# Kernel optimization log

Measured on AMD Instinct MI355X. Metric: run time of the kernel, lower is better.

## Reference

```python
import jax, jax.numpy as jnp
import numpy as np

N_HEAD = 16
N_KV_HEAD = 4
HEAD_DIM = 128
RMS_EPS = 1.1920928955078125e-07  # torch float32 eps used by F.rms_norm default


def apply_rotary_emb(x, cos, sin):
    # x: [B,T,H,D]; cos/sin: [1,T,1,D/2]
    d = x.shape[-1] // 2
    x1, x2 = x[..., :d], x[..., d:]
    return jnp.concatenate([x1 * cos + x2 * sin, -x1 * sin + x2 * cos], axis=-1)


def rms_norm(x):
    return x * jax.lax.rsqrt(jnp.mean(x * x, axis=-1, keepdims=True) + RMS_EPS)


def setup_inputs() -> dict:
    key = jax.random.key(0)
    ks = jax.random.split(key, 7)
    B, T, C = 2, 2048, 2048
    return {
        "x": jax.random.normal(ks[0], (B, T, C), jnp.float32),
        "cos": jax.random.normal(ks[1], (1, T, 1, HEAD_DIM // 2), jnp.float32),
        "sin": jax.random.normal(ks[2], (1, T, 1, HEAD_DIM // 2), jnp.float32),
        "wq": jax.random.normal(ks[3], (C, N_HEAD * HEAD_DIM), jnp.float32) * 0.02,
        "wk": jax.random.normal(ks[4], (C, N_KV_HEAD * HEAD_DIM), jnp.float32) * 0.02,
        "wv": jax.random.normal(ks[5], (C, N_KV_HEAD * HEAD_DIM), jnp.float32) * 0.02,
        "wo": jax.random.normal(ks[6], (C, C), jnp.float32) * 0.02,
        "window_size": 512,
    }


def reference(x, cos, sin, wq, wk, wv, wo, window_size):
    B, T, C = x.shape
    H, KV, D = N_HEAD, N_KV_HEAD, HEAD_DIM
    rep = H // KV
    q = (x @ wq).reshape(B, T, H, D)
    k = (x @ wk).reshape(B, T, KV, D)
    v = (x @ wv).reshape(B, T, KV, D)
    q = rms_norm(apply_rotary_emb(q, cos, sin))
    k = rms_norm(apply_rotary_emb(k, cos, sin))
    # GQA: group query heads by kv head instead of materializing expanded K/V
    qg = q.reshape(B, T, KV, rep, D)
    scale = 1.0 / np.sqrt(D)
    scores = jnp.einsum('btkrd,bskd->bkrts', qg, k) * scale  # [B,KV,rep,T,S]
    row = jnp.arange(T)[:, None]
    col = jnp.arange(T)[None, :]
    mask = (col <= row) & (row - col <= window_size)  # causal & sliding window
    scores = jnp.where(mask, scores, jnp.finfo(scores.dtype).min)
    probs = jax.nn.softmax(scores, axis=-1)
    y = jnp.einsum('bkrts,bskd->btkrd', probs, v).reshape(B, T, H * D)
    return y @ wo
```

## Files before the change

kernel.cpp:

```cpp
#include <hip/hip_runtime.h>
#include <stdint.h>

typedef __attribute__((ext_vector_type(4))) float f32x4;
typedef __attribute__((ext_vector_type(8))) __bf16 bf16x8;
typedef __attribute__((ext_vector_type(4))) unsigned int u32x4;
typedef unsigned short u16;

#define B_DIM 2
#define T_DIM 2048
#define C_DIM 2048
#define H_Q   16
#define H_KV  4
#define HD    128
#define NQKV  3072
#define MTOK  4096
#define RMS_EPS 1.1920928955078125e-07f

__device__ __forceinline__ u16 f2bf(float f) {
  union { float f; unsigned int u; } v; v.f = f;
  unsigned int r = v.u + 0x7FFFu + ((v.u >> 16) & 1u);
  return (u16)(r >> 16);
}
__device__ __forceinline__ float bf2f(u16 h) {
  union { unsigned int u; float f; } v; v.u = ((unsigned int)h) << 16;
  return v.f;
}
__device__ __forceinline__ f32x4 mfma16(bf16x8 a, bf16x8 b, f32x4 c) {
  return __builtin_amdgcn_mfma_f32_16x16x32_bf16(a, b, c, 0, 0, 0);
}
__device__ __forceinline__ void gl_lds16(const void* g, void* l) {
  __builtin_amdgcn_global_load_lds(
      (const __attribute__((address_space(1))) unsigned int*)g,
      (__attribute__((address_space(3))) unsigned int*)l, 16, 0, 0);
}

__global__ __launch_bounds__(256) void prep_kernel(const float* __restrict__ x,
                                                   const float* __restrict__ wq,
                                                   const float* __restrict__ wk,
                                                   const float* __restrict__ wv,
                                                   const float* __restrict__ wo,
                                                   u16* __restrict__ xb,
                                                   u16* __restrict__ wqkvb,
                                                   u16* __restrict__ wob) {
  __shared__ float tile[64][65];
  int bid = blockIdx.x, t = threadIdx.x;
  if (bid < 2560) {
    int nb = bid % 80, kb = bid / 80;
    const float* src; u16* dst; int srcN, nloc;
    if (nb < 32)      { src = wq; srcN = 2048; nloc = nb;      dst = wqkvb; }
    else if (nb < 40) { src = wk; srcN = 512;  nloc = nb - 32; dst = wqkvb + (size_t)2048 * 2048; }
    else if (nb < 48) { src = wv; srcN = 512;  nloc = nb - 40; dst = wqkvb + (size_t)2560 * 2048; }
    else              { src = wo; srcN = 2048; nloc = nb - 48; dst = wob; }
    int n0 = nloc * 64, k0 = kb * 64;
    #pragma unroll
    for (int idx = t; idx < 4096; idx += 256) {
      int r = idx >> 6, c = idx & 63;
      tile[r][c] = src[(size_t)(k0 + r) * srcN + n0 + c];
    }
    __syncthreads();
    #pragma unroll
    for (int idx = t; idx < 4096; idx += 256) {
      int r = idx >> 6, c = idx & 63;
      dst[(size_t)(n0 + r) * 2048 + k0 + c] = f2bf(tile[c][r]);
    }
  } else {
    int i = ((bid - 2560) * 256 + t) * 4;
    if (i >= MTOK * C_DIM) return;
    float4 v = *(const float4*)(x + i);
    u16 o0 = f2bf(v.x), o1 = f2bf(v.y), o2 = f2bf(v.z), o3 = f2bf(v.w);
    unsigned int lo = (unsigned int)o0 | ((unsigned int)o1 << 16);
    unsigned int hi = (unsigned int)o2 | ((unsigned int)o3 << 16);
    *(uint2*)(xb + i) = make_uint2(lo, hi);
  }
}

__global__ __launch_bounds__(256) void ropevt_kernel(u16* __restrict__ qkv,
                                                     const float* __restrict__ cosb,
                                                     const float* __restrict__ sinb,
                                                     u16* __restrict__ vt) {
  __shared__ __align__(16) u16 tile[64][136];
  int bid = blockIdx.x, tid = threadIdx.x;
  if (bid < 256) {
    int tt0 = (bid & 31) * 64;
    int kvh = (bid >> 5) & 3;
    int b   = bid >> 7;
    const u16* vp = qkv + ((size_t)b * T_DIM + tt0) * NQKV + C_DIM + H_KV * HD + kvh * HD;
    #pragma unroll
    for (int i = 0; i < 4; ++i) {
      int cid = tid + i * 256;
      int r = cid >> 4, c = cid & 15;
      u32x4 v = *(const u32x4*)(vp + (size_t)r * NQKV + c * 8);
      *(u32x4*)&tile[r][c * 8] = v;
    }
    __syncthreads();
    u16* op = vt + ((size_t)(b * H_KV + kvh) * HD) * T_DIM + tt0;
    #pragma unroll
    for (int i = 0; i < 4; ++i) {
      int cid = tid + i * 256;
      int d = cid >> 3, tc = cid & 7;
      u16 vals[8];
      #pragma unroll
      for (int j = 0; j < 8; ++j) vals[j] = tile[tc * 8 + j][d];
      u32x4 w;
      w.x = (unsigned int)vals[0] | ((unsigned int)vals[1] << 16);
      w.y = (unsigned int)vals[2] | ((unsigned int)vals[3] << 16);
      w.z = (unsigned int)vals[4] | ((unsigned int)vals[5] << 16);
      w.w = (unsigned int)vals[6] | ((unsigned int)vals[7] << 16);
      *(u32x4*)(op + (size_t)d * T_DIM + tc * 8) = w;
    }
  } else {
    int gw = ((bid - 256) * 256 + tid) >> 6;
    int lane = tid & 63;
    int hh = gw % (H_Q + H_KV);
    int tok = gw / (H_Q + H_KV);
    int t = tok & (T_DIM - 1);
    int base = (hh < H_Q) ? hh * HD : (C_DIM + (hh - H_Q) * HD);
    u16* p = qkv + (size_t)tok * NQKV + base;
    float x1 = bf2f(p[lane]);
    float x2 = bf2f(p[lane + 64]);
    float c = cosb[t * 64 + lane];
    float s = sinb[t * 64 + lane];
    float o1 =  x1 * c + x2 * s;
    float o2 = -x1 * s + x2 * c;
    float ss = o1 * o1 + o2 * o2;
    #pragma unroll
    for (int off = 1; off < 64; off <<= 1) ss += __shfl_xor(ss, off);
    float r = rsqrtf(ss * (1.0f / 128.0f) + RMS_EPS);
    p[lane]      = f2bf(o1 * r);
    p[lane + 64] = f2bf(o2 * r);
  }
}

template<int BF16OUT>
__global__ __launch_bounds__(256) void gemm_bt_kernel(const u16* __restrict__ A,
                                                      const u16* __restrict__ Bt,
                                                      void* __restrict__ Cv,
                                                      int M, int N, int K) {
  __shared__ __align__(16) u16 Asm[128 * 64];
  __shared__ __align__(16) u16 Bsm[128 * 64];
  const int tid = threadIdx.x;
  const int lane = tid & 63;
  const int wid = tid >> 6;
  const int m0 = blockIdx.y * 128, n0 = blockIdx.x * 128;
  const int wm = (wid >> 1) * 64, wn = (wid & 1) * 64;
  const int l15 = lane & 15, l4 = lane >> 4;
  const int csrc = (lane & 7) ^ (lane >> 3);
  f32x4 acc[4][4] = {};

  for (int k0 = 0; k0 < K; k0 += 64) {
    __syncthreads();
    #pragma unroll
    for (int i = 0; i < 4; ++i) {
      int g = wid * 4 + i;
      int row = g * 8 + (lane >> 3);
      gl_lds16(A  + (size_t)(m0 + row) * K + k0 + csrc * 8, (char*)Asm + g * 1024);
      gl_lds16(Bt + (size_t)(n0 + row) * K + k0 + csrc * 8, (char*)Bsm + g * 1024);
    }
    __syncthreads();
    #pragma unroll
    for (int ks = 0; ks < 2; ++ks) {
      bf16x8 af[4], bfr[4];
      #pragma unroll
      for (int mf = 0; mf < 4; ++mf) {
        int r = wm + mf * 16 + l15;
        int bo = r * 128 + (((ks * 4 + l4) ^ (r & 7)) * 16);
        af[mf] = __builtin_bit_cast(bf16x8, *(const u32x4*)((const char*)Asm + bo));
      }
      #pragma unroll
      for (int nf = 0; nf < 4; ++nf) {
        int r = wn + nf * 16 + l15;
        int bo = r * 128 + (((ks * 4 + l4) ^ (r & 7)) * 16);
        bfr[nf] = __builtin_bit_cast(bf16x8, *(const u32x4*)((const char*)Bsm + bo));
      }
      #pragma unroll
      for (int mf = 0; mf < 4; ++mf)
        #pragma unroll
        for (int nf = 0; nf < 4; ++nf)
          acc[mf][nf] = mfma16(af[mf], bfr[nf], acc[mf][nf]);
    }
  }
  #pragma unroll
  for (int mf = 0; mf < 4; ++mf)
    #pragma unroll
    for (int nf = 0; nf < 4; ++nf)
      #pragma unroll
      for (int reg = 0; reg < 4; ++reg) {
        int row = m0 + wm + mf * 16 + l4 * 4 + reg;
        int col = n0 + wn + nf * 16 + l15;
        float v = acc[mf][nf][reg];
        if (BF16OUT) ((u16*)Cv)[(size_t)row * N + col] = f2bf(v);
        else         ((float*)Cv)[(size_t)row * N + col] = v;
      }
}

__global__ __launch_bounds__(256) void attn_kernel(const u16* __restrict__ qkv,
                                                   const u16* __restrict__ vt,
                                                   u16* __restrict__ yb,
                                                   const int* __restrict__ wsz_p) {
  __shared__ __align__(16) u16 Ksm[2][64 * 128];
  __shared__ __align__(16) u16 Vsm[2][128 * 64];
  __shared__ __align__(16) u16 Psm[4 * 16 * 64];

  const int W = wsz_p[0];
  const int tid = threadIdx.x, lane = tid & 63, wid = tid >> 6;
  const int l15 = lane & 15, l4 = lane >> 4;
  const int bid = blockIdx.x;
  const int h   = bid & 15;
  const int b   = (bid >> 4) & 1;
  const int qt  = 31 - (bid >> 5);
  const int kvh = h >> 2;
  const size_t tokb = (size_t)b * T_DIM;
  const u16* vtb = vt + ((size_t)(b * H_KV + kvh) * HD) * T_DIM;
  const int rbase = qt * 64 + wid * 16;

  const int krow4 = wid * 16 + ((lane >> 4) | ((lane & 15) << 28) * 0);
  auto stage = [&](int kt, int bufsel) {
    const u16* kp = qkv + (tokb + kt * 64) * NQKV + C_DIM + kvh * HD;
    #pragma unroll
    for (int i = 0; i < 4; ++i) {
      int g = wid * 4 + i;
      int row = g * 4 + (lane >> 4);
      int cs = (lane & 15) ^ (row & 15);
      gl_lds16(kp + (size_t)row * NQKV + cs * 8, (char*)Ksm[bufsel] + g * 1024);
    }
    const u16* vp = vtb + kt * 64;
    #pragma unroll
    for (int i = 0; i < 4; ++i) {
      int g = wid * 4 + i;
      int d = g * 8 + (lane >> 3);
      int cs = (lane & 7) ^ (d & 7);
      gl_lds16(vp + (size_t)d * T_DIM + cs * 8, (char*)Vsm[bufsel] + g * 1024);
    }
  };

  bf16x8 qf[4];
  {
    int r = rbase + l15;
    const u16* qp = qkv + (tokb + r) * NQKV + h * HD;
    #pragma unroll
    for (int ks = 0; ks < 4; ++ks)
      qf[ks] = __builtin_bit_cast(bf16x8, *(const u32x4*)(qp + ks * 32 + l4 * 8));
  }

  f32x4 yacc[8] = {};
  float mrow[4], lrow[4];
  #pragma unroll
  for (int rg = 0; rg < 4; ++rg) { mrow[rg] = -3.0e38f; lrow[rg] = 0.0f; }

  const float sc = 0.08838834764831845f * 1.4426950408889634f;
  int smin = qt * 64 - W; if (smin < 0) smin = 0;
  const int t0 = smin >> 6;
  char* pbase = (char*)Psm + wid * 2048;

  stage(t0, 0);
  __syncthreads();
  int cur = 0;

  for (int kt = t0; kt <= qt; ++kt) {
    if (kt < qt) stage(kt + 1, cur ^ 1);

    const int slo = kt * 64;
    bool active = (slo <= rbase + 15) && ((rbase - (slo + 63)) <= W);
    if (active) {
      float Sc[4][4];
      #pragma unroll
      for (int nf = 0; nf < 4; ++nf) {
        f32x4 sa = {0.f, 0.f, 0.f, 0.f};
        int key = nf * 16 + l15;
        #pragma unroll
        for (int ks = 0; ks < 4; ++ks) {
          int bo = key * 256 + (((ks * 4 + l4) ^ (key & 15)) * 16);
          bf16x8 kf = __builtin_bit_cast(bf16x8, *(const u32x4*)((const char*)Ksm[cur] + bo));
          sa = mfma16(qf[ks], kf, sa);
        }
        #pragma unroll
        for (int rg = 0; rg < 4; ++rg) Sc[nf][rg] = sa[rg] * sc;
      }
      bool fullvalid = ((slo + 63) <= rbase) && ((rbase + 15 - slo) <= W);
      if (!fullvalid) {
        #pragma unroll
        for (int nf = 0; nf < 4; ++nf) {
          int s = slo + nf * 16 + l15;
          #pragma unroll
          for (int rg = 0; rg < 4; ++rg) {
            int r = rbase + l4 * 4 + rg;
            if (s > r || (r - s) > W) Sc[nf][rg] = -3.0e38f;
          }
        }
      }
      float fmul[4];
      #pragma unroll
      for (int rg = 0; rg < 4; ++rg) {
        float tm = fmaxf(fmaxf(Sc[0][rg], Sc[1][rg]), fmaxf(Sc[2][rg], Sc[3][rg]));
        #pragma unroll
        for (int off = 1; off < 16; off <<= 1) tm = fmaxf(tm, __shfl_xor(tm, off));
        float mnew = fmaxf(mrow[rg], tm);
        float mo = fmaxf(mrow[rg], -1.0e30f);
        float mc = fmaxf(mnew,     -1.0e30f);
        fmul[rg] = exp2f(mo - mc);
        mrow[rg] = mnew;
      }
      float rs[4] = {0.f, 0.f, 0.f, 0.f};
      #pragma unroll
      for (int nf = 0; nf < 4; ++nf)
        #pragma unroll
        for (int rg = 0; rg < 4; ++rg) {
          float mc = fmaxf(mrow[rg], -1.0e30f);
          float pv = exp2f(Sc[nf][rg] - mc);
          rs[rg] += pv;
          int q   = l4 * 4 + rg;
          int key = nf * 16 + l15;
          int bo = q * 128 + (((key >> 3) ^ (q & 7)) * 16) + (key & 7) * 2;
          *(u16*)(pbase + bo) = f2bf(pv);
        }
      #pragma unroll
      for (int rg = 0; rg < 4; ++rg) {
        #pragma unroll
        for (int off = 1; off < 16; off <<= 1) rs[rg] += __shfl_xor(rs[rg], off);
        lrow[rg] = lrow[rg] * fmul[rg] + rs[rg];
      }
      f32x4 fv = {fmul[0], fmul[1], fmul[2], fmul[3]};
      #pragma unroll
      for (int nf2 = 0; nf2 < 8; ++nf2) yacc[nf2] *= fv;

      #pragma unroll
      for (int ks2 = 0; ks2 < 2; ++ks2) {
        int boA = l15 * 128 + (((ks2 * 4 + l4) ^ (l15 & 7)) * 16);
        bf16x8 pa = __builtin_bit_cast(bf16x8, *(const u32x4*)(pbase + boA));
        #pragma unroll
        for (int nf2 = 0; nf2 < 8; ++nf2) {
          int d = nf2 * 16 + l15;
          int boB = d * 128 + (((ks2 * 4 + l4) ^ (d & 7)) * 16);
          bf16x8 vf = __builtin_bit_cast(bf16x8, *(const u32x4*)((const char*)Vsm[cur] + boB));
          yacc[nf2] = mfma16(pa, vf, yacc[nf2]);
        }
      }
    }
    __syncthreads();
    cur ^= 1;
  }

  #pragma unroll
  for (int nf2 = 0; nf2 < 8; ++nf2)
    #pragma unroll
    for (int rg = 0; rg < 4; ++rg) {
      int r = rbase + l4 * 4 + rg;
      float v = yacc[nf2][rg] / lrow[rg];
      yb[(tokb + r) * (size_t)C_DIM + h * HD + nf2 * 16 + l15] = f2bf(v);
    }
}

extern "C" void kernel_launch(void* const* d_in, const int* in_sizes, int n_in,
                              void* d_out, int out_size, void* d_ws, size_t ws_size,
                              hipStream_t stream) {
  const float* x    = (const float*)d_in[0];
  const float* cosb = (const float*)d_in[1];
  const float* sinb = (const float*)d_in[2];
  const float* wq   = (const float*)d_in[3];
  const float* wk   = (const float*)d_in[4];
  const float* wv   = (const float*)d_in[5];
  const float* wo   = (const float*)d_in[6];
  const int*   wsz  = (const int*)d_in[7];

  char* ws = (char*)d_ws;
  u16* xb    = (u16*)(ws);
  u16* qkvb  = (u16*)(ws + (size_t)16777216);
  u16* wqkvb = (u16*)(ws + (size_t)41943040);
  u16* wob   = (u16*)(ws + (size_t)54525952);
  u16* ybuf  = (u16*)(ws + (size_t)62914560);
  u16* vtb   = (u16*)(ws);

  prep_kernel<<<2560 + 8192, 256, 0, stream>>>(x, wq, wk, wv, wo, xb, wqkvb, wob);
  gemm_bt_kernel<1><<<dim3(NQKV / 128, MTOK / 128), 256, 0, stream>>>(xb, wqkvb, qkvb, MTOK, NQKV, C_DIM);
  ropevt_kernel<<<256 + (MTOK * (H_Q + H_KV)) / 4, 256, 0, stream>>>(qkvb, cosb, sinb, vtb);
  attn_kernel<<<B_DIM * H_Q * (T_DIM / 64), 256, 0, stream>>>(qkvb, vtb, ybuf, wsz);
  gemm_bt_kernel<0><<<dim3(C_DIM / 128, MTOK / 128), 256, 0, stream>>>(ybuf, wob, d_out, MTOK, C_DIM, C_DIM);
}
```

Before: 191.8 us.

## Fold softmax scale into Q norm, lazy rescale, truncate P to bf16

Folds the 1/sqrt(D)*log2(e) softmax scale into the Q RMS-norm epilogue, so the attention loop no longer multiplies scores. It adds a lazy online-softmax rescale: the running max and the accumulator are only updated when some row's tile max exceeds the old max by more than 8 (in log2 units), with the skip decided per wavefront. It also replaces round-to-nearest bf16 conversion of P with truncation, and sums the truncated values into the row sum so the numerator and denominator stay consistent. Together these trim VALU work in the softmax inner loop. The cost is slightly different numerics from truncation and from exponents up to 2^8 before normalisation.

Result: no change. 193.1 us (+0.7%).

```diff
diff --git a/kernel.cpp b/kernel.cpp
--- a/kernel.cpp
+++ b/kernel.cpp
@@ -15,6 +15,7 @@
 #define NQKV  3072
 #define MTOK  4096
 #define RMS_EPS 1.1920928955078125e-07f
+#define Q_SCALE 0.12751749f
 
 __device__ __forceinline__ u16 f2bf(float f) {
   union { float f; unsigned int u; } v; v.f = f;
@@ -114,7 +115,8 @@
     int hh = gw % (H_Q + H_KV);
     int tok = gw / (H_Q + H_KV);
     int t = tok & (T_DIM - 1);
-    int base = (hh < H_Q) ? hh * HD : (C_DIM + (hh - H_Q) * HD);
+    bool isq = (hh < H_Q);
+    int base = isq ? hh * HD : (C_DIM + (hh - H_Q) * HD);
     u16* p = qkv + (size_t)tok * NQKV + base;
     float x1 = bf2f(p[lane]);
     float x2 = bf2f(p[lane + 64]);
@@ -126,6 +128,7 @@
     #pragma unroll
     for (int off = 1; off < 64; off <<= 1) ss += __shfl_xor(ss, off);
     float r = rsqrtf(ss * (1.0f / 128.0f) + RMS_EPS);
+    if (isq) r *= Q_SCALE;
     p[lane]      = f2bf(o1 * r);
     p[lane + 64] = f2bf(o2 * r);
   }
@@ -213,7 +216,6 @@
   const u16* vtb = vt + ((size_t)(b * H_KV + kvh) * HD) * T_DIM;
   const int rbase = qt * 64 + wid * 16;
 
-  const int krow4 = wid * 16 + ((lane >> 4) | ((lane & 15) << 28) * 0);
   auto stage = [&](int kt, int bufsel) {
     const u16* kp = qkv + (tokb + kt * 64) * NQKV + C_DIM + kvh * HD;
     #pragma unroll
@@ -247,7 +249,6 @@
   #pragma unroll
   for (int rg = 0; rg < 4; ++rg) { mrow[rg] = -3.0e38f; lrow[rg] = 0.0f; }
 
-  const float sc = 0.08838834764831845f * 1.4426950408889634f;
   int smin = qt * 64 - W; if (smin < 0) smin = 0;
   const int t0 = smin >> 6;
   char* pbase = (char*)Psm + wid * 2048;
@@ -274,7 +275,7 @@
           sa = mfma16(qf[ks], kf, sa);
         }
         #pragma unroll
-        for (int rg = 0; rg < 4; ++rg) Sc[nf][rg] = sa[rg] * sc;
+        for (int rg = 0; rg < 4; ++rg) Sc[nf][rg] = sa[rg];
       }
       bool fullvalid = ((slo + 63) <= rbase) && ((rbase + 15 - slo) <= W);
       if (!fullvalid) {
@@ -288,40 +289,51 @@
           }
         }
       }
-      float fmul[4];
+      float tmax[4];
       #pragma unroll
       for (int rg = 0; rg < 4; ++rg) {
         float tm = fmaxf(fmaxf(Sc[0][rg], Sc[1][rg]), fmaxf(Sc[2][rg], Sc[3][rg]));
         #pragma unroll
         for (int off = 1; off < 16; off <<= 1) tm = fmaxf(tm, __shfl_xor(tm, off));
-        float mnew = fmaxf(mrow[rg], tm);
-        float mo = fmaxf(mrow[rg], -1.0e30f);
-        float mc = fmaxf(mnew,     -1.0e30f);
-        fmul[rg] = exp2f(mo - mc);
-        mrow[rg] = mnew;
-      }
+        tmax[rg] = tm;
+      }
+      bool small = tmax[0] <= mrow[0] + 8.f && tmax[1] <= mrow[1] + 8.f &&
+                   tmax[2] <= mrow[2] + 8.f && tmax[3] <= mrow[3] + 8.f;
+      if (!__all(small)) {
+        f32x4 fv;
+        #pragma unroll
+        for (int rg = 0; rg < 4; ++rg) {
+          float mnew = fmaxf(mrow[rg], tmax[rg]);
+          float fm = exp2f(fmaxf(mrow[rg], -1.0e30f) - fmaxf(mnew, -1.0e30f));
+          mrow[rg] = mnew;
+          fv[rg] = fm;
+          lrow[rg] *= fm;
+        }
+        #pragma unroll
+        for (int nf2 = 0; nf2 < 8; ++nf2) yacc[nf2] *= fv;
+      }
+      float mc[4];
+      #pragma unroll
+      for (int rg = 0; rg < 4; ++rg) mc[rg] = fmaxf(mrow[rg], -1.0e30f);
       float rs[4] = {0.f, 0.f, 0.f, 0.f};
       #pragma unroll
       for (int nf = 0; nf < 4; ++nf)
         #pragma unroll
         for (int rg = 0; rg < 4; ++rg) {
-          float mc = fmaxf(mrow[rg], -1.0e30f);
-          float pv = exp2f(Sc[nf][rg] - mc);
-          rs[rg] += pv;
+          float pv = exp2f(Sc[nf][rg] - mc[rg]);
+          unsigned int pbits = __builtin_bit_cast(unsigned int, pv);
+          rs[rg] += __builtin_bit_cast(float, pbits & 0xFFFF0000u);
           int q   = l4 * 4 + rg;
           int key = nf * 16 + l15;
           int bo = q * 128 + (((key >> 3) ^ (q & 7)) * 16) + (key & 7) * 2;
-          *(u16*)(pbase + bo) = f2bf(pv);
+          *(u16*)(pbase + bo) = (u16)(pbits >> 16);
         }
       #pragma unroll
       for (int rg = 0; rg < 4; ++rg) {
         #pragma unroll
         for (int off = 1; off < 16; off <<= 1) rs[rg] += __shfl_xor(rs[rg], off);
-        lrow[rg] = lrow[rg] * fmul[rg] + rs[rg];
-      }
-      f32x4 fv = {fmul[0], fmul[1], fmul[2], fmul[3]};
-      #pragma unroll
-      for (int nf2 = 0; nf2 < 8; ++nf2) yacc[nf2] *= fv;
+        lrow[rg] += rs[rg];
+      }
 
       #pragma unroll
       for (int ks2 = 0; ks2 < 2; ++ks2) {
```
